# Kernel optimization log

Hardware: AMD Instinct MI355X
Metric: run time of the kernel (lower is better)

The kernel has to match this reference:

```python
import jax, jax.numpy as jnp
import numpy as np

N_NODES = 50000

def sage_conv(x, src, dst, W_l, b_l, W_r):
    # mean-aggregate neighbor features x[src] at dst, then lin_l(agg)+lin_r(x)
    msgs = x[src]                                       # [E, d]
    agg = jax.ops.segment_sum(msgs, dst, num_segments=N_NODES)
    cnt = jax.ops.segment_sum(jnp.ones((src.shape[0],), x.dtype), dst, num_segments=N_NODES)
    agg = agg / jnp.maximum(cnt, 1.0)[:, None]          # [N, d]
    return agg @ W_l.T + b_l + x @ W_r.T


def setup_inputs() -> dict:
    key = jax.random.key(0)
    ks = jax.random.split(key, 10)
    in_c, hid, out_c = 128, 128, 64
    x = jax.random.normal(ks[0], (N_NODES, in_c), dtype=jnp.float32)
    edge_index = jax.random.randint(ks[1], (2, 800000), 0, N_NODES, dtype=jnp.int64)
    s = 1.0 / np.sqrt(in_c)
    W1_l = jax.random.uniform(ks[2], (hid, in_c), minval=-s, maxval=s)
    b1 = jax.random.uniform(ks[3], (hid,), minval=-s, maxval=s)
    W1_r = jax.random.uniform(ks[4], (hid, in_c), minval=-s, maxval=s)
    s = 1.0 / np.sqrt(hid)
    W2_l = jax.random.uniform(ks[5], (hid, hid), minval=-s, maxval=s)
    b2 = jax.random.uniform(ks[6], (hid,), minval=-s, maxval=s)
    W2_r = jax.random.uniform(ks[7], (hid, hid), minval=-s, maxval=s)
    W3 = jax.random.uniform(ks[8], (out_c, hid), minval=-s, maxval=s)
    b3 = jax.random.uniform(ks[9], (out_c,), minval=-s, maxval=s)
    return {"x": x, "edge_index": edge_index, "W1_l": W1_l, "b1": b1, "W1_r": W1_r,
            "W2_l": W2_l, "b2": b2, "W2_r": W2_r, "W3": W3, "b3": b3}


def reference(x, edge_index, W1_l, b1, W1_r, W2_l, b2, W2_r, W3, b3):
    src, dst = edge_index[0], edge_index[1]
    h = jax.nn.relu(sage_conv(x, src, dst, W1_l, b1, W1_r))
    h = jax.nn.relu(sage_conv(h, src, dst, W2_l, b2, W2_r))
    return h @ W3.T + b3
```

## Files before the change

kernel.cpp:

```cpp
#include <hip/hip_runtime.h>

#define FDIM 128

typedef __attribute__((ext_vector_type(8))) short bf16x8;
typedef __attribute__((ext_vector_type(4))) float f32x4;

static __device__ __forceinline__ ushort f2bf(float f) {
    uint u = __float_as_uint(f);
    uint r = (u + 0x7FFF + ((u >> 16) & 1)) >> 16;
    return (ushort)r;
}
static __device__ __forceinline__ uint packbf(float lo, float hi) {
    return (uint)f2bf(lo) | ((uint)f2bf(hi) << 16);
}
static __device__ __forceinline__ float bflo(uint v) { return __uint_as_float(v << 16); }
static __device__ __forceinline__ float bfhi(uint v) { return __uint_as_float(v & 0xFFFF0000u); }

#define ACC8(A, V) do { \
    A[0] += bflo((V).x); A[1] += bfhi((V).x); \
    A[2] += bflo((V).y); A[3] += bfhi((V).y); \
    A[4] += bflo((V).z); A[5] += bfhi((V).z); \
    A[6] += bflo((V).w); A[7] += bfhi((V).w); } while (0)


__global__ void prep_kernel(const float* __restrict__ x, ushort* __restrict__ xb, int nx8,
                            const float* __restrict__ W1l, const float* __restrict__ W1r,
                            const float* __restrict__ W2l, const float* __restrict__ W2r,
                            const float* __restrict__ W3, ushort* __restrict__ wbuf,
                            const int* __restrict__ dst, int E, int* __restrict__ bcnt,
                            int* __restrict__ hdone, int* __restrict__ bbase,
                            int* __restrict__ bcur, int nb, int nconv, int nhist) {
    const int b = blockIdx.x;
    const int tid = threadIdx.x;
    if (b < nconv) {
        int i = b * 256 + tid;
        if (i < nx8) {
            const float* s = x + (size_t)i * 8;
            float4 a = *(const float4*)(s);
            float4 c = *(const float4*)(s + 4);
            uint4 o;
            o.x = packbf(a.x, a.y); o.y = packbf(a.z, a.w);
            o.z = packbf(c.x, c.y); o.w = packbf(c.z, c.w);
            *(uint4*)(xb + (size_t)i * 8) = o;
        }
    } else if (b < nconv + 36) {
        int c = (b - nconv) * 256 + tid;
        const float* s; ushort* d;
        if (c < 2048)      { s = W1l + (size_t)c * 8;          d = wbuf + (size_t)c * 8; }
        else if (c < 4096) { s = W1r + (size_t)(c - 2048) * 8; d = wbuf + 16384 + (size_t)(c - 2048) * 8; }
        else if (c < 6144) { s = W2l + (size_t)(c - 4096) * 8; d = wbuf + 32768 + (size_t)(c - 4096) * 8; }
        else if (c < 8192) { s = W2r + (size_t)(c - 6144) * 8; d = wbuf + 49152 + (size_t)(c - 6144) * 8; }
        else               { s = W3  + (size_t)(c - 8192) * 8; d = wbuf + 65536 + (size_t)(c - 8192) * 8; }
        float4 a = *(const float4*)(s);
        float4 cc = *(const float4*)(s + 4);
        uint4 o;
        o.x = packbf(a.x, a.y); o.y = packbf(a.z, a.w);
        o.z = packbf(cc.x, cc.y); o.w = packbf(cc.z, cc.w);
        *(uint4*)d = o;
    } else {
        __shared__ int lh[256];
        __shared__ int isLast;
        int hb = b - nconv - 36;
        lh[tid] = 0;
        __syncthreads();
        #pragma unroll
        for (int k = 0; k < 8; ++k) {
            int e = hb * 2048 + k * 256 + tid;
            if (e < E) atomicAdd(&lh[dst[e] >> 8], 1);
        }
        __syncthreads();
        if (lh[tid]) atomicAdd(&bcnt[tid], lh[tid]);
        __syncthreads();
        if (tid == 0) {
            __threadfence();
            isLast = (atomicAdd(hdone, 1) == nhist - 1);
        }
        __syncthreads();
        if (isLast && tid < 64) {
            __threadfence();
            volatile int* vb = bcnt;
            const int i0 = tid * 4;
            int v0 = (i0 + 0 < nb) ? vb[i0 + 0] : 0;
            int v1 = (i0 + 1 < nb) ? vb[i0 + 1] : 0;
            int v2 = (i0 + 2 < nb) ? vb[i0 + 2] : 0;
            int v3 = (i0 + 3 < nb) ? vb[i0 + 3] : 0;
            int s = v0 + v1 + v2 + v3;
            int incl = s;
            #pragma unroll
            for (int d = 1; d < 64; d <<= 1) {
                int t = __shfl_up(incl, d);
                if (tid >= d) incl += t;
            }
            int excl = incl - s;
            int e0 = excl, e1 = excl + v0, e2 = e1 + v1, e3 = e2 + v2;
            if (i0 + 0 < nb) { bbase[i0 + 0] = e0; bcur[i0 + 0] = e0; }
            if (i0 + 1 < nb) { bbase[i0 + 1] = e1; bcur[i0 + 1] = e1; }
            if (i0 + 2 < nb) { bbase[i0 + 2] = e2; bcur[i0 + 2] = e2; }
            if (i0 + 3 < nb) { bbase[i0 + 3] = e3; bcur[i0 + 3] = e3; }
            int total = __shfl(incl, 63);
            if (tid == 0) bbase[nb] = total;
        }
    }
}


__global__ void pair_scatter(const int* __restrict__ src, const int* __restrict__ dst,
                             int* __restrict__ bcur, uint* __restrict__ pairs, int E) {
    __shared__ int lh[256];
    __shared__ int gb[256];
    const int tid = threadIdx.x;
    lh[tid] = 0;
    __syncthreads();
    int ss[8], dd[8], sl[8];
    #pragma unroll
    for (int k = 0; k < 8; ++k) {
        int e = blockIdx.x * 2048 + k * 256 + tid;
        if (e < E) {
            ss[k] = src[e];
            dd[k] = dst[e];
            sl[k] = atomicAdd(&lh[dd[k] >> 8], 1);
        } else dd[k] = -1;
    }
    __syncthreads();
    if (lh[tid]) gb[tid] = atomicAdd(&bcur[tid], lh[tid]);
    __syncthreads();
    #pragma unroll
    for (int k = 0; k < 8; ++k) {
        if (dd[k] >= 0)
            pairs[gb[dd[k] >> 8] + sl[k]] = (uint)ss[k] | ((uint)(dd[k] & 255) << 24);
    }
}


__global__ void bucket_csr(const uint* __restrict__ pairs, const int* __restrict__ bbase,
                           int* __restrict__ off, int* __restrict__ csr, int N) {
    __shared__ int cnt[256];
    __shared__ int base[256];
    __shared__ int cur[256];
    const int b = blockIdx.x;
    const int tid = threadIdx.x;
    const int p0 = bbase[b], p1 = bbase[b + 1];
    cnt[tid] = 0;
    __syncthreads();
    for (int p = p0 + tid; p < p1; p += 256) atomicAdd(&cnt[pairs[p] >> 24], 1);
    __syncthreads();
    if (tid < 64) {
        int i0 = tid * 4;
        int v0 = cnt[i0], v1 = cnt[i0 + 1], v2 = cnt[i0 + 2], v3 = cnt[i0 + 3];
        int s = v0 + v1 + v2 + v3;
        int incl = s;
        #pragma unroll
        for (int d = 1; d < 64; d <<= 1) {
            int t = __shfl_up(incl, d);
            if (tid >= d) incl += t;
        }
        int excl = incl - s;
        base[i0] = excl; base[i0 + 1] = excl + v0;
        base[i0 + 2] = excl + v0 + v1; base[i0 + 3] = excl + v0 + v1 + v2;
        cur[i0] = base[i0]; cur[i0 + 1] = base[i0 + 1];
        cur[i0 + 2] = base[i0 + 2]; cur[i0 + 3] = base[i0 + 3];
    }
    __syncthreads();
    int node = (b << 8) + tid;
    if (node <= N) off[node] = p0 + base[tid];
    for (int p = p0 + tid; p < p1; p += 256) {
        uint e = pairs[p];
        int slot = atomicAdd(&cur[e >> 24], 1);
        csr[p0 + slot] = (int)(e & 0xFFFFFF);
    }
}


#define PS 132

template<int HEAD>
__global__ __launch_bounds__(256, 8)
void fused_sage(const ushort* __restrict__ feat, const int* __restrict__ off,
                const int* __restrict__ csr,
                const ushort* __restrict__ Wl, const ushort* __restrict__ Wr,
                const float* __restrict__ bias,
                const ushort* __restrict__ W3, const float* __restrict__ b3,
                ushort* __restrict__ hout, float* __restrict__ fout, int n) {
    __shared__ __align__(16) ushort As[16 * FDIM];
    __shared__ __align__(16) ushort Xs[16 * FDIM];
    __shared__ __align__(16) float psum[16 * PS];
    const int row0 = blockIdx.x * 16;
    const int lane = threadIdx.x & 63;
    const int wid  = threadIdx.x >> 6;

    {
        int r = threadIdx.x >> 4, cch = threadIdx.x & 15;
        int row = row0 + r;
        float4 vx = make_float4(0.f, 0.f, 0.f, 0.f);
        if (row < n) vx = *(const float4*)(feat + (size_t)row * FDIM + cch * 8);
        *(float4*)(Xs + (r * 16 + (cch ^ (r & 7))) * 8) = vx;
    }

    const int g = lane >> 4;
    const int c = lane & 15;
    #define LDROW(s) (*(const uint4*)(feat + (size_t)(s) * FDIM + c * 8))
    for (int i = 0; i < 4; ++i) {
        const int r = wid * 4 + i;
        const int node = row0 + r;
        float a[8] = {0.f, 0.f, 0.f, 0.f, 0.f, 0.f, 0.f, 0.f};
        float inv = 0.f;
        if (node < n) {
            const int j0 = off[node], j1 = off[node + 1];
            int j = j0 + g;
            for (; j + 12 < j1; j += 16) {
                int s0 = csr[j], s1 = csr[j + 4], s2 = csr[j + 8], s3 = csr[j + 12];
                uint4 v0 = LDROW(s0), v1 = LDROW(s1), v2 = LDROW(s2), v3 = LDROW(s3);
                ACC8(a, v0); ACC8(a, v1); ACC8(a, v2); ACC8(a, v3);
            }
            for (; j + 4 < j1; j += 8) {
                int s0 = csr[j], s1 = csr[j + 4];
                uint4 v0 = LDROW(s0), v1 = LDROW(s1);
                ACC8(a, v0); ACC8(a, v1);
            }
            for (; j < j1; j += 4) {
                uint4 v0 = LDROW(csr[j]);
                ACC8(a, v0);
            }
            inv = 1.0f / fmaxf((float)(j1 - j0), 1.0f);
        }
        #pragma unroll
        for (int k = 0; k < 8; ++k) {
            a[k] += __shfl_xor(a[k], 16);
            a[k] += __shfl_xor(a[k], 32);
        }
        if (g == 0) {
            uint4 o;
            o.x = packbf(a[0] * inv, a[1] * inv);
            o.y = packbf(a[2] * inv, a[3] * inv);
            o.z = packbf(a[4] * inv, a[5] * inv);
            o.w = packbf(a[6] * inv, a[7] * inv);
            *(uint4*)(As + (r * 16 + (c ^ (r & 7))) * 8) = o;
        }
    }
    #undef LDROW
    __syncthreads();

    const int op   = wid >> 1;
    const int half = wid & 1;
    const int lr = lane & 15;
    const int lk = lane >> 4;
    const ushort* Atile = op ? Xs : As;
    const ushort* W     = op ? Wr : Wl;

    f32x4 acc[4];
    #pragma unroll
    for (int t = 0; t < 4; ++t) acc[t] = (f32x4){0.f, 0.f, 0.f, 0.f};

    #pragma unroll
    for (int ks = 0; ks < 4; ++ks) {
        bf16x8 a = *(const bf16x8*)(Atile + (lr * 16 + ((ks * 4 + lk) ^ (lr & 7))) * 8);
        #pragma unroll
        for (int t = 0; t < 4; ++t) {
            int wr = half * 64 + t * 16 + lr;
            bf16x8 bb = *(const bf16x8*)(W + (size_t)wr * FDIM + ks * 32 + lk * 8);
            acc[t] = __builtin_amdgcn_mfma_f32_16x16x32_bf16(a, bb, acc[t], 0, 0, 0);
        }
    }

    if (op == 1) {
        #pragma unroll
        for (int t = 0; t < 4; ++t) {
            #pragma unroll
            for (int j = 0; j < 4; ++j)
                psum[(lk * 4 + j) * PS + half * 64 + t * 16 + lr] = acc[t][j];
        }
    }
    __syncthreads();

    if (op == 0) {
        #pragma unroll
        for (int t = 0; t < 4; ++t) {
            int col = half * 64 + t * 16 + lr;
            float bc = bias[col];
            #pragma unroll
            for (int j = 0; j < 4; ++j) {
                int r = lk * 4 + j;
                float v = fmaxf(acc[t][j] + psum[r * PS + col] + bc, 0.f);
                if (HEAD == 0) {
                    int row = row0 + r;
                    if (row < n) hout[(size_t)row * FDIM + col] = f2bf(v);
                } else {
                    As[(r * 16 + ((col >> 3) ^ (r & 7))) * 8 + (col & 7)] = f2bf(v);
                }
            }
        }
    }

    if (HEAD == 1) {
        __syncthreads();
        f32x4 acc2 = (f32x4){0.f, 0.f, 0.f, 0.f};
        #pragma unroll
        for (int ks = 0; ks < 4; ++ks) {
            bf16x8 a = *(const bf16x8*)(As + (lr * 16 + ((ks * 4 + lk) ^ (lr & 7))) * 8);
            int wr = wid * 16 + lr;
            bf16x8 bb = *(const bf16x8*)(W3 + (size_t)wr * FDIM + ks * 32 + lk * 8);
            acc2 = __builtin_amdgcn_mfma_f32_16x16x32_bf16(a, bb, acc2, 0, 0, 0);
        }
        int col = wid * 16 + lr;
        float bc = b3[col];
        #pragma unroll
        for (int j = 0; j < 4; ++j) {
            int row = row0 + lk * 4 + j;
            if (row < n) fout[(size_t)row * 64 + col] = acc2[j] + bc;
        }
    }
}


extern "C" void kernel_launch(void* const* d_in, const int* in_sizes, int n_in,
                              void* d_out, int out_size, void* d_ws, size_t ws_size,
                              hipStream_t stream) {
    const float* x   = (const float*)d_in[0];
    const int*   ei  = (const int*)d_in[1];
    const float* W1l = (const float*)d_in[2];
    const float* b1  = (const float*)d_in[3];
    const float* W1r = (const float*)d_in[4];
    const float* W2l = (const float*)d_in[5];
    const float* b2  = (const float*)d_in[6];
    const float* W2r = (const float*)d_in[7];
    const float* W3  = (const float*)d_in[8];
    const float* b3  = (const float*)d_in[9];
    float* out = (float*)d_out;

    const int N = in_sizes[0] / FDIM;
    const int E = in_sizes[1] / 2;
    const int* src = ei;
    const int* dst = ei + E;
    const int NBK = (N + 255) >> 8;

    char* ws = (char*)d_ws;
    size_t p = 0;
    auto alloc = [&](size_t bytes) {
        char* q = ws + p;
        p += (bytes + 255) & ~(size_t)255;
        return q;
    };
    int* ctrl    = (int*)alloc(272 * 4);
    int* bcnt    = ctrl;
    int* hdone   = ctrl + 256;
    int* bbase   = (int*)alloc(260 * 4);
    int* bcur    = (int*)alloc(256 * 4);
    uint* pairs  = (uint*)alloc((size_t)E * 4);
    int* csr     = (int*)alloc((size_t)E * 4);
    int* off     = (int*)alloc((size_t)(N + 1) * 4);
    ushort* xb   = (ushort*)alloc((size_t)N * FDIM * 2);
    ushort* h1b  = (ushort*)alloc((size_t)N * FDIM * 2);
    ushort* wbuf = (ushort*)alloc(73728 * 2);
    ushort* w1l = wbuf, *w1r = wbuf + 16384, *w2l = wbuf + 32768,
           *w2r = wbuf + 49152, *w3 = wbuf + 65536;

    hipMemsetAsync(ctrl, 0, 257 * 4, stream);

    const int nx8   = N * FDIM / 8;
    const int nconv = (nx8 + 255) / 256;
    const int nhist = (E + 2047) / 2048;
    prep_kernel<<<nconv + 36 + nhist, 256, 0, stream>>>(
        x, xb, nx8, W1l, W1r, W2l, W2r, W3, wbuf, dst, E, bcnt,
        hdone, bbase, bcur, NBK, nconv, nhist);
    pair_scatter<<<(E + 2047) / 2048, 256, 0, stream>>>(src, dst, bcur, pairs, E);
    bucket_csr<<<NBK, 256, 0, stream>>>(pairs, bbase, off, csr, N);

    const int lgrid = (N + 15) / 16;
    fused_sage<0><<<lgrid, 256, 0, stream>>>(xb, off, csr, w1l, w1r, b1,
                                             (const ushort*)nullptr, (const float*)nullptr,
                                             h1b, (float*)nullptr, N);
    fused_sage<1><<<lgrid, 256, 0, stream>>>(h1b, off, csr, w2l, w2r, b2,
                                             w3, b3, (ushort*)nullptr, out, N);
}
```

Before: 171.8 us.

## Gather neighbor features in FP8 while keeping bf16 copy for self term

Node features are now stored twice, as bf16 for the self/root linear term and as FP8 (e4m3) for the neighbor gather. The edge aggregation loop reads 8-byte FP8 rows and converts them with packed hardware conversion instructions. This halves the bytes moved in the random-access gather, which dominates traffic. In exchange the aggregation loses precision, and extra FP8 copies must be written in prep and in the first layer's output, the latter with byte-granular scalar stores.

```diff
diff --git a/kernel.cpp b/kernel.cpp
--- a/kernel.cpp
+++ b/kernel.cpp
@@ -4,6 +4,7 @@
 
 typedef __attribute__((ext_vector_type(8))) short bf16x8;
 typedef __attribute__((ext_vector_type(4))) float f32x4;
+typedef __attribute__((ext_vector_type(2))) float f32x2;
 
 static __device__ __forceinline__ ushort f2bf(float f) {
     uint u = __float_as_uint(f);
@@ -13,17 +14,25 @@
 static __device__ __forceinline__ uint packbf(float lo, float hi) {
     return (uint)f2bf(lo) | ((uint)f2bf(hi) << 16);
 }
-static __device__ __forceinline__ float bflo(uint v) { return __uint_as_float(v << 16); }
-static __device__ __forceinline__ float bfhi(uint v) { return __uint_as_float(v & 0xFFFF0000u); }
-
-#define ACC8(A, V) do { \
-    A[0] += bflo((V).x); A[1] += bfhi((V).x); \
-    A[2] += bflo((V).y); A[3] += bfhi((V).y); \
-    A[4] += bflo((V).z); A[5] += bfhi((V).z); \
-    A[6] += bflo((V).w); A[7] += bfhi((V).w); } while (0)
-
-
-__global__ void prep_kernel(const float* __restrict__ x, ushort* __restrict__ xb, int nx8,
+static __device__ __forceinline__ uint pk8(float a, float b, float c, float d) {
+    uint u = __builtin_amdgcn_cvt_pk_fp8_f32(a, b, 0, false);
+    return __builtin_amdgcn_cvt_pk_fp8_f32(c, d, u, true);
+}
+static __device__ __forceinline__ uchar pk1(float v) {
+    return (uchar)(__builtin_amdgcn_cvt_pk_fp8_f32(v, v, 0, false) & 0xFF);
+}
+
+#define ACCF8(A, V) do { \
+    f32x2 p0 = __builtin_amdgcn_cvt_pk_f32_fp8((V).x, false); \
+    f32x2 p1 = __builtin_amdgcn_cvt_pk_f32_fp8((V).x, true);  \
+    f32x2 p2 = __builtin_amdgcn_cvt_pk_f32_fp8((V).y, false); \
+    f32x2 p3 = __builtin_amdgcn_cvt_pk_f32_fp8((V).y, true);  \
+    A[0] += p0.x; A[1] += p0.y; A[2] += p1.x; A[3] += p1.y;   \
+    A[4] += p2.x; A[5] += p2.y; A[6] += p3.x; A[7] += p3.y; } while (0)
+
+
+__global__ void prep_kernel(const float* __restrict__ x, ushort* __restrict__ xbn,
+                            uchar* __restrict__ xf8, int nx8,
                             const float* __restrict__ W1l, const float* __restrict__ W1r,
                             const float* __restrict__ W2l, const float* __restrict__ W2r,
                             const float* __restrict__ W3, ushort* __restrict__ wbuf,
@@ -41,7 +50,11 @@
             uint4 o;
             o.x = packbf(a.x, a.y); o.y = packbf(a.z, a.w);
             o.z = packbf(c.x, c.y); o.w = packbf(c.z, c.w);
-            *(uint4*)(xb + (size_t)i * 8) = o;
+            *(uint4*)(xbn + (size_t)i * 8) = o;
+            uint2 q;
+            q.x = pk8(a.x, a.y, a.z, a.w);
+            q.y = pk8(c.x, c.y, c.z, c.w);
+            *(uint2*)(xf8 + (size_t)i * 8) = q;
         }
     } else if (b < nconv + 36) {
         int c = (b - nconv) * 256 + tid;
@@ -175,12 +188,13 @@
 
 template<int HEAD>
 __global__ __launch_bounds__(256, 8)
-void fused_sage(const ushort* __restrict__ feat, const int* __restrict__ off,
-                const int* __restrict__ csr,
+void fused_sage(const uchar* __restrict__ feat8, const ushort* __restrict__ featn,
+                const int* __restrict__ off, const int* __restrict__ csr,
                 const ushort* __restrict__ Wl, const ushort* __restrict__ Wr,
                 const float* __restrict__ bias,
                 const ushort* __restrict__ W3, const float* __restrict__ b3,
-                ushort* __restrict__ hout, float* __restrict__ fout, int n) {
+                ushort* __restrict__ houtn, uchar* __restrict__ hout8,
+                float* __restrict__ fout, int n) {
     __shared__ __align__(16) ushort As[16 * FDIM];
     __shared__ __align__(16) ushort Xs[16 * FDIM];
     __shared__ __align__(16) float psum[16 * PS];
@@ -192,13 +206,13 @@
         int r = threadIdx.x >> 4, cch = threadIdx.x & 15;
         int row = row0 + r;
         float4 vx = make_float4(0.f, 0.f, 0.f, 0.f);
-        if (row < n) vx = *(const float4*)(feat + (size_t)row * FDIM + cch * 8);
+        if (row < n) vx = *(const float4*)(featn + (size_t)row * FDIM + cch * 8);
         *(float4*)(Xs + (r * 16 + (cch ^ (r & 7))) * 8) = vx;
     }
 
     const int g = lane >> 4;
     const int c = lane & 15;
-    #define LDROW(s) (*(const uint4*)(feat + (size_t)(s) * FDIM + c * 8))
+    #define LDROW(s) (*(const uint2*)(feat8 + (size_t)(s) * FDIM + c * 8))
     for (int i = 0; i < 4; ++i) {
         const int r = wid * 4 + i;
         const int node = row0 + r;
@@ -209,17 +223,17 @@
             int j = j0 + g;
             for (; j + 12 < j1; j += 16) {
                 int s0 = csr[j], s1 = csr[j + 4], s2 = csr[j + 8], s3 = csr[j + 12];
-                uint4 v0 = LDROW(s0), v1 = LDROW(s1), v2 = LDROW(s2), v3 = LDROW(s3);
-                ACC8(a, v0); ACC8(a, v1); ACC8(a, v2); ACC8(a, v3);
+                uint2 v0 = LDROW(s0), v1 = LDROW(s1), v2 = LDROW(s2), v3 = LDROW(s3);
+                ACCF8(a, v0); ACCF8(a, v1); ACCF8(a, v2); ACCF8(a, v3);
             }
             for (; j + 4 < j1; j += 8) {
                 int s0 = csr[j], s1 = csr[j + 4];
-                uint4 v0 = LDROW(s0), v1 = LDROW(s1);
-                ACC8(a, v0); ACC8(a, v1);
+                uint2 v0 = LDROW(s0), v1 = LDROW(s1);
+                ACCF8(a, v0); ACCF8(a, v1);
             }
             for (; j < j1; j += 4) {
-                uint4 v0 = LDROW(csr[j]);
-                ACC8(a, v0);
+                uint2 v0 = LDROW(csr[j]);
+                ACCF8(a, v0);
             }
             inv = 1.0f / fmaxf((float)(j1 - j0), 1.0f);
         }
@@ -283,7 +297,10 @@
                 float v = fmaxf(acc[t][j] + psum[r * PS + col] + bc, 0.f);
                 if (HEAD == 0) {
                     int row = row0 + r;
-                    if (row < n) hout[(size_t)row * FDIM + col] = f2bf(v);
+                    if (row < n) {
+                        houtn[(size_t)row * FDIM + col] = f2bf(v);
+                        hout8[(size_t)row * FDIM + col] = pk1(v);
+                    }
                 } else {
                     As[(r * 16 + ((col >> 3) ^ (r & 7))) * 8 + (col & 7)] = f2bf(v);
                 }
@@ -348,8 +365,10 @@
     uint* pairs  = (uint*)alloc((size_t)E * 4);
     int* csr     = (int*)alloc((size_t)E * 4);
     int* off     = (int*)alloc((size_t)(N + 1) * 4);
-    ushort* xb   = (ushort*)alloc((size_t)N * FDIM * 2);
-    ushort* h1b  = (ushort*)alloc((size_t)N * FDIM * 2);
+    ushort* xbn  = (ushort*)alloc((size_t)N * FDIM * 2);
+    uchar*  xf8  = (uchar*)alloc((size_t)N * FDIM);
+    ushort* h1n  = (ushort*)alloc((size_t)N * FDIM * 2);
+    uchar*  h1f8 = (uchar*)alloc((size_t)N * FDIM);
     ushort* wbuf = (ushort*)alloc(73728 * 2);
     ushort* w1l = wbuf, *w1r = wbuf + 16384, *w2l = wbuf + 32768,
            *w2r = wbuf + 49152, *w3 = wbuf + 65536;
@@ -360,15 +379,15 @@
     const int nconv = (nx8 + 255) / 256;
     const int nhist = (E + 2047) / 2048;
     prep_kernel<<<nconv + 36 + nhist, 256, 0, stream>>>(
-        x, xb, nx8, W1l, W1r, W2l, W2r, W3, wbuf, dst, E, bcnt,
+        x, xbn, xf8, nx8, W1l, W1r, W2l, W2r, W3, wbuf, dst, E, bcnt,
         hdone, bbase, bcur, NBK, nconv, nhist);
     pair_scatter<<<(E + 2047) / 2048, 256, 0, stream>>>(src, dst, bcur, pairs, E);
     bucket_csr<<<NBK, 256, 0, stream>>>(pairs, bbase, off, csr, N);
 
     const int lgrid = (N + 15) / 16;
-    fused_sage<0><<<lgrid, 256, 0, stream>>>(xb, off, csr, w1l, w1r, b1,
+    fused_sage<0><<<lgrid, 256, 0, stream>>>(xf8, xbn, off, csr, w1l, w1r, b1,
                                              (const ushort*)nullptr, (const float*)nullptr,
-                                             h1b, (float*)nullptr, N);
-    fused_sage<1><<<lgrid, 256, 0, stream>>>(h1b, off, csr, w2l, w2r, b2,
-                                             w3, b3, (ushort*)nullptr, out, N);
-}
+                                             h1n, h1f8, (float*)nullptr, N);
+    fused_sage<1><<<lgrid, 256, 0, stream>>>(h1f8, h1n, off, csr, w2l, w2r, b2,
+                                             w3, b3, (ushort*)nullptr, (uchar*)nullptr, out, N);
+}
```

After: 166.0 us. 3.3% less time.
